# Kernel optimization log

Measured on AMD Instinct MI355X. Metric: run time of the kernel, lower is better.

## Reference

```python
import jax, jax.numpy as jnp
import numpy as np

B, T, D, KDIM = 256, 512, 256, 256

def setup_inputs() -> dict:
    key = jax.random.key(0)
    k1, k2, k3 = jax.random.split(key, 3)
    inputs = jax.random.normal(k1, (B, T, D), dtype=jnp.float32)
    # glorot-style scaling for stability of the recurrence
    U = jax.random.normal(k2, (D, KDIM), dtype=jnp.float32) * (1.0 / np.sqrt(D))
    W = jax.random.normal(k3, (KDIM, KDIM), dtype=jnp.float32) * (1.0 / np.sqrt(KDIM))
    b = jnp.zeros((KDIM,), dtype=jnp.float32)
    return {"inputs": inputs, "U": U, "W": W, "b": b}

def reference(inputs, U, W, b):
    # vanilla RNN: h_t = tanh(x_t U + h_{t-1} W + b); returns final hidden state
    xU = jnp.einsum('btd,dk->btk', inputs, U) + b  # precompute input projection [B,T,K]

    def step(h, xu_t):
        h = jnp.tanh(xu_t + h @ W)
        return h, None

    h0 = jnp.zeros((inputs.shape[0], W.shape[0]), dtype=inputs.dtype)
    h_final, _ = jax.lax.scan(step, h0, jnp.swapaxes(xU, 0, 1))  # scan over time
    # original keras code keeps a singleton time axis on the state: [B,1,K]
    return h_final[:, None, :]
```

## Files before the change

### kernel.cpp

```cpp
#include <hip/hip_runtime.h>
#include <hip/hip_bf16.h>


typedef _Float16 half8_t __attribute__((ext_vector_type(8)));
typedef _Float16 half2_t __attribute__((ext_vector_type(2)));
typedef float    float4_t __attribute__((ext_vector_type(4)));

#define MFMA16(a, b, c) __builtin_amdgcn_mfma_f32_16x16x32_f16((a), (b), (c), 0, 0, 0)

__device__ __forceinline__ half2_t pk_h2(float a, float b) {
    auto r = __builtin_amdgcn_cvt_pkrtz(a, b);
    return __builtin_bit_cast(half2_t, r);
}

__device__ __forceinline__ float fast_tanh(float x) {
    float e = __builtin_amdgcn_exp2f(2.8853900817779268f * x);
    return 1.0f - 2.0f * __builtin_amdgcn_rcpf(e + 1.0f);
}

__device__ __forceinline__ void lds_barrier() {
    __builtin_amdgcn_sched_barrier(0);
    asm volatile("s_waitcnt lgkmcnt(0)" ::: "memory");
    __builtin_amdgcn_s_barrier();
    __builtin_amdgcn_sched_barrier(0);
}

__global__ void transpose_u(const float* __restrict__ U, _Float16* __restrict__ Ut) {
    int id = blockIdx.x * 256 + threadIdx.x;
    int d = id >> 8, n = id & 255;
    Ut[n * 264 + d] = (_Float16)U[id];
}

__global__ __launch_bounds__(256, 3) void xu_gemm(
    const float* __restrict__ x,
    const _Float16* __restrict__ Ut,
    const float* __restrict__ bias,
    half2_t* __restrict__ xu)
{
    __shared__ char lds[40960];
    const int tid = threadIdx.x;
    const int lane = tid & 63, w = tid >> 6, l15 = lane & 15, q = lane >> 4;
    const int bx = blockIdx.x;
    const int m_tile = (bx & 7) | ((bx >> 4) << 3);
    const int n0 = ((bx >> 3) & 1) * 128;
    const size_t m0 = (size_t)m_tile * 128;

    float4 ar[4];
    uint4  br[2];

    auto loadA = [&](int it) {
#pragma unroll
        for (int i = 0; i < 4; ++i) {
            int u = tid + 256 * i, row = u >> 3, seg = u & 7;
            ar[i] = *(const float4*)(x + (m0 + row) * 256 + it * 32 + seg * 4);
        }
    };
    auto loadB = [&](int it) {
#pragma unroll
        for (int i = 0; i < 2; ++i) {
            int u = tid + 256 * i, p = u >> 2, seg = u & 3;
            int c = n0 + 32 * (p >> 5) + 2 * (p & 15) + ((p >> 4) & 1);
            br[i] = *(const uint4*)((const char*)Ut + c * 528 + it * 64 + seg * 16);
        }
    };
    auto writeAB = [&](int s) {
        char* As = lds + s * 10240;
        char* Bs = lds + 20480 + s * 10240;
#pragma unroll
        for (int i = 0; i < 4; ++i) {
            int u = tid + 256 * i, row = u >> 3, seg = u & 7;
            half2_t p0 = pk_h2(ar[i].x, ar[i].y);
            half2_t p1 = pk_h2(ar[i].z, ar[i].w);
            uint2 v;
            v.x = __builtin_bit_cast(unsigned, p0);
            v.y = __builtin_bit_cast(unsigned, p1);
            *(uint2*)(As + row * 80 + seg * 8) = v;
        }
#pragma unroll
        for (int i = 0; i < 2; ++i) {
            int u = tid + 256 * i, p = u >> 2, seg = u & 3;
            *(uint4*)(Bs + p * 80 + seg * 16) = br[i];
        }
    };

    float4_t acc[16];
#pragma unroll
    for (int i = 0; i < 16; ++i) { acc[i][0] = 0.f; acc[i][1] = 0.f; acc[i][2] = 0.f; acc[i][3] = 0.f; }

    loadA(0); loadB(0); writeAB(0);
    __syncthreads();

    for (int it = 0; it < 8; ++it) {
        if (it < 7) { loadA(it + 1); loadB(it + 1); }
        const char* As = lds + (it & 1) * 10240;
        const char* Bs = lds + 20480 + (it & 1) * 10240;
        half8_t af[2];
#pragma unroll
        for (int ms = 0; ms < 2; ++ms)
            af[ms] = *(const half8_t*)(As + (32 * w + 16 * ms + l15) * 80 + q * 16);
#pragma unroll
        for (int ns = 0; ns < 8; ++ns) {
            half8_t bf = *(const half8_t*)(Bs + (16 * ns + l15) * 80 + q * 16);
            acc[ns * 2 + 0] = MFMA16(af[0], bf, acc[ns * 2 + 0]);
            acc[ns * 2 + 1] = MFMA16(af[1], bf, acc[ns * 2 + 1]);
        }
        if (it < 7) writeAB((it + 1) & 1);
        __syncthreads();
    }

#pragma unroll
    for (int ms = 0; ms < 2; ++ms)
#pragma unroll
        for (int j = 0; j < 4; ++j) {
            const int c = n0 + 32 * j + 2 * l15;
            const float2 bb = *(const float2*)(bias + c);
#pragma unroll
            for (int i = 0; i < 4; ++i) {
                float v0 = acc[(2 * j) * 2 + ms][i] + bb.x;
                float v1 = acc[(2 * j + 1) * 2 + ms][i] + bb.y;
                half2_t p = pk_h2(v0, v1);
                int m_g = (int)m0 + 32 * w + 16 * ms + q * 4 + i;
                xu[(size_t)m_g * 128 + (c >> 1)] = p;
            }
        }
}

__global__ __launch_bounds__(512, 2) void rnn_scan(
    const half2_t* __restrict__ xu,
    const float* __restrict__ W,
    float* __restrict__ out)
{
    __shared__ char lds[16896];
    const int tid = threadIdx.x;
    const int lane = tid & 63, w = tid >> 6, l15 = lane & 15, q = lane >> 4;
    const int blk = blockIdx.x;
    const int c0 = 32 * w + 2 * l15;

    half8_t wf[2][8];
#pragma unroll
    for (int tt = 0; tt < 2; ++tt)
#pragma unroll
        for (int c = 0; c < 8; ++c) {
            half8_t f;
#pragma unroll
            for (int j = 0; j < 8; ++j) {
                int k = 32 * c + q * 8 + j;
                f[j] = (_Float16)W[k * 256 + c0 + tt];
            }
            wf[tt][c] = f;
        }

    for (int i = tid; i < 16896 / 4; i += 512) ((int*)lds)[i] = 0;

    const int rowg0 = 16 * blk + q * 4;
    const int colh = c0 >> 1;

    unsigned xoff[4];
#pragma unroll
    for (int i = 0; i < 4; ++i)
        xoff[i] = (unsigned)(rowg0 + i) * 512u * 128u + (unsigned)colh;

    half2_t xr[4][4];
#pragma unroll
    for (int p = 0; p < 4; ++p)
#pragma unroll
        for (int i = 0; i < 4; ++i)
            xr[p][i] = xu[xoff[i] + (unsigned)p * 128u];
#pragma unroll
    for (int i = 0; i < 4; ++i) xoff[i] += 512u;

    char* const L = (char*)lds;
    const int afb = l15 * 528 + q * 16;
    const int hwb = (q * 4) * 528 + c0 * 2;

    __syncthreads();

#define SCAN_STEP(P_, PAR, DOPF, LAST)                                          \
    {                                                                           \
        const char* hcur = L + ((PAR) ? 8448 : 0);                              \
        half8_t af[8];                                                          \
        _Pragma("unroll")                                                       \
        for (int c8 = 0; c8 < 8; ++c8)                                          \
            af[c8] = *(const half8_t*)(hcur + afb + c8 * 64);                   \
        float4_t a0a, a1a, a0b, a1b;                                            \
        _Pragma("unroll")                                                       \
        for (int i = 0; i < 4; ++i) {                                           \
            a0a[i] = (float)xr[P_][i][0];                                       \
            a1a[i] = (float)xr[P_][i][1];                                       \
            a0b[i] = 0.f; a1b[i] = 0.f;                                         \
        }                                                                       \
        if (DOPF) {                                                             \
            _Pragma("unroll")                                                   \
            for (int i = 0; i < 4; ++i) {                                       \
                xr[P_][i] = xu[xoff[i]];                                        \
                xoff[i] += 128u;                                                \
            }                                                                   \
        }                                                                       \
        _Pragma("unroll")                                                       \
        for (int c = 0; c < 4; ++c) {                                           \
            a0a = MFMA16(af[2 * c],     wf[0][2 * c],     a0a);                 \
            a1a = MFMA16(af[2 * c],     wf[1][2 * c],     a1a);                 \
            a0b = MFMA16(af[2 * c + 1], wf[0][2 * c + 1], a0b);                 \
            a1b = MFMA16(af[2 * c + 1], wf[1][2 * c + 1], a1b);                 \
        }                                                                       \
        if (LAST) {                                                             \
            _Pragma("unroll")                                                   \
            for (int i = 0; i < 4; ++i) {                                       \
                float2 st;                                                      \
                st.x = fast_tanh(a0a[i] + a0b[i]);                              \
                st.y = fast_tanh(a1a[i] + a1b[i]);                              \
                *(float2*)(&out[(rowg0 + i) * 256 + c0]) = st;                  \
            }                                                                   \
        } else {                                                                \
            char* hnext = L + ((PAR) ? 0 : 8448);                               \
            _Pragma("unroll")                                                   \
            for (int i = 0; i < 4; ++i) {                                       \
                float v0 = fast_tanh(a0a[i] + a0b[i]);                          \
                float v1 = fast_tanh(a1a[i] + a1b[i]);                          \
                *(half2_t*)(hnext + hwb + i * 528) = pk_h2(v0, v1);             \
            }                                                                   \
            lds_barrier();                                                      \
        }                                                                       \
    }

    for (int t4 = 0; t4 < 508; t4 += 4) {
        SCAN_STEP(0, 0, 1, 0)
        SCAN_STEP(1, 1, 1, 0)
        SCAN_STEP(2, 0, 1, 0)
        SCAN_STEP(3, 1, 1, 0)
    }
    SCAN_STEP(0, 0, 0, 0)
    SCAN_STEP(1, 1, 0, 0)
    SCAN_STEP(2, 0, 0, 0)
    SCAN_STEP(3, 1, 0, 1)
#undef SCAN_STEP
}

extern "C" void kernel_launch(void* const* d_in, const int* in_sizes, int n_in,
                              void* d_out, int out_size, void* d_ws, size_t ws_size,
                              hipStream_t stream) {
    const float* x = (const float*)d_in[0];
    const float* U = (const float*)d_in[1];
    const float* W = (const float*)d_in[2];
    const float* b = (const float*)d_in[3];
    float* out = (float*)d_out;

    char* ws = (char*)d_ws;
    _Float16* Ut = (_Float16*)ws;
    half2_t*  xu = (half2_t*)(ws + 262144);

    transpose_u<<<256, 256, 0, stream>>>(U, Ut);
    xu_gemm<<<2048, 256, 0, stream>>>(x, Ut, b, xu);
    rnn_scan<<<16, 512, 0, stream>>>(xu, W, out);
}
```

Measured before the change: 523.4 us.

## Fuse projection GEMM and RNN scan into one kernel with flag-based time-chunk overlap

Merges the U transpose, the xU projection GEMM and the recurrent scan into a single persistent launch. Blocks 0-15 run the scan while the remaining blocks compute xU in time-quarter chunks, publishing progress through global atomic flags so the scan can start once the first quarter is ready. The GEMM blocks now cover 128 rows x 256 columns each, sharing one A tile across two 256-thread halves. The aim is to hide the GEMM and launch gaps behind the serial scan, at the cost of spin-wait synchronisation and a reliance on all blocks being co-resident or scheduled in order to avoid deadlock.

```diff
diff --git a/kernel.cpp b/kernel.cpp
--- a/kernel.cpp
+++ b/kernel.cpp
@@ -25,155 +25,91 @@
     __builtin_amdgcn_sched_barrier(0);
 }
 
-__global__ void transpose_u(const float* __restrict__ U, _Float16* __restrict__ Ut) {
-    int id = blockIdx.x * 256 + threadIdx.x;
-    int d = id >> 8, n = id & 255;
-    Ut[n * 264 + d] = (_Float16)U[id];
-}
-
-__global__ __launch_bounds__(256, 3) void xu_gemm(
+__device__ __forceinline__ void wait_flag(unsigned* f, unsigned target) {
+    if (threadIdx.x == 0) {
+        while (__hip_atomic_load(f, __ATOMIC_ACQUIRE, __HIP_MEMORY_SCOPE_AGENT) < target)
+            __builtin_amdgcn_s_sleep(16);
+    }
+    __builtin_amdgcn_sched_barrier(0);
+    __builtin_amdgcn_s_barrier();
+    __builtin_amdgcn_sched_barrier(0);
+    asm volatile("" ::: "memory");
+}
+
+__global__ __launch_bounds__(512, 2) void fused(
     const float* __restrict__ x,
-    const _Float16* __restrict__ Ut,
+    const float* __restrict__ U,
+    const float* __restrict__ W,
     const float* __restrict__ bias,
-    half2_t* __restrict__ xu)
-{
-    __shared__ char lds[40960];
-    const int tid = threadIdx.x;
-    const int lane = tid & 63, w = tid >> 6, l15 = lane & 15, q = lane >> 4;
-    const int bx = blockIdx.x;
-    const int m_tile = (bx & 7) | ((bx >> 4) << 3);
-    const int n0 = ((bx >> 3) & 1) * 128;
-    const size_t m0 = (size_t)m_tile * 128;
-
-    float4 ar[4];
-    uint4  br[2];
-
-    auto loadA = [&](int it) {
-#pragma unroll
-        for (int i = 0; i < 4; ++i) {
-            int u = tid + 256 * i, row = u >> 3, seg = u & 7;
-            ar[i] = *(const float4*)(x + (m0 + row) * 256 + it * 32 + seg * 4);
-        }
-    };
-    auto loadB = [&](int it) {
-#pragma unroll
-        for (int i = 0; i < 2; ++i) {
-            int u = tid + 256 * i, p = u >> 2, seg = u & 3;
-            int c = n0 + 32 * (p >> 5) + 2 * (p & 15) + ((p >> 4) & 1);
-            br[i] = *(const uint4*)((const char*)Ut + c * 528 + it * 64 + seg * 16);
-        }
-    };
-    auto writeAB = [&](int s) {
-        char* As = lds + s * 10240;
-        char* Bs = lds + 20480 + s * 10240;
-#pragma unroll
-        for (int i = 0; i < 4; ++i) {
-            int u = tid + 256 * i, row = u >> 3, seg = u & 7;
-            half2_t p0 = pk_h2(ar[i].x, ar[i].y);
-            half2_t p1 = pk_h2(ar[i].z, ar[i].w);
-            uint2 v;
-            v.x = __builtin_bit_cast(unsigned, p0);
-            v.y = __builtin_bit_cast(unsigned, p1);
-            *(uint2*)(As + row * 80 + seg * 8) = v;
-        }
-#pragma unroll
-        for (int i = 0; i < 2; ++i) {
-            int u = tid + 256 * i, p = u >> 2, seg = u & 3;
-            *(uint4*)(Bs + p * 80 + seg * 16) = br[i];
-        }
-    };
-
-    float4_t acc[16];
-#pragma unroll
-    for (int i = 0; i < 16; ++i) { acc[i][0] = 0.f; acc[i][1] = 0.f; acc[i][2] = 0.f; acc[i][3] = 0.f; }
-
-    loadA(0); loadB(0); writeAB(0);
-    __syncthreads();
-
-    for (int it = 0; it < 8; ++it) {
-        if (it < 7) { loadA(it + 1); loadB(it + 1); }
-        const char* As = lds + (it & 1) * 10240;
-        const char* Bs = lds + 20480 + (it & 1) * 10240;
-        half8_t af[2];
-#pragma unroll
-        for (int ms = 0; ms < 2; ++ms)
-            af[ms] = *(const half8_t*)(As + (32 * w + 16 * ms + l15) * 80 + q * 16);
-#pragma unroll
-        for (int ns = 0; ns < 8; ++ns) {
-            half8_t bf = *(const half8_t*)(Bs + (16 * ns + l15) * 80 + q * 16);
-            acc[ns * 2 + 0] = MFMA16(af[0], bf, acc[ns * 2 + 0]);
-            acc[ns * 2 + 1] = MFMA16(af[1], bf, acc[ns * 2 + 1]);
-        }
-        if (it < 7) writeAB((it + 1) & 1);
-        __syncthreads();
-    }
-
-#pragma unroll
-    for (int ms = 0; ms < 2; ++ms)
-#pragma unroll
-        for (int j = 0; j < 4; ++j) {
-            const int c = n0 + 32 * j + 2 * l15;
-            const float2 bb = *(const float2*)(bias + c);
-#pragma unroll
-            for (int i = 0; i < 4; ++i) {
-                float v0 = acc[(2 * j) * 2 + ms][i] + bb.x;
-                float v1 = acc[(2 * j + 1) * 2 + ms][i] + bb.y;
-                half2_t p = pk_h2(v0, v1);
-                int m_g = (int)m0 + 32 * w + 16 * ms + q * 4 + i;
-                xu[(size_t)m_g * 128 + (c >> 1)] = p;
-            }
-        }
-}
-
-__global__ __launch_bounds__(512, 2) void rnn_scan(
-    const half2_t* __restrict__ xu,
-    const float* __restrict__ W,
+    _Float16* __restrict__ Ut,
+    half2_t* __restrict__ xu,
+    unsigned* __restrict__ flags,
     float* __restrict__ out)
 {
-    __shared__ char lds[16896];
+    __shared__ char lds[61440];
     const int tid = threadIdx.x;
-    const int lane = tid & 63, w = tid >> 6, l15 = lane & 15, q = lane >> 4;
-    const int blk = blockIdx.x;
-    const int c0 = 32 * w + 2 * l15;
-
-    half8_t wf[2][8];
-#pragma unroll
-    for (int tt = 0; tt < 2; ++tt)
-#pragma unroll
-        for (int c = 0; c < 8; ++c) {
-            half8_t f;
-#pragma unroll
-            for (int j = 0; j < 8; ++j) {
-                int k = 32 * c + q * 8 + j;
-                f[j] = (_Float16)W[k * 256 + c0 + tt];
-            }
-            wf[tt][c] = f;
-        }
-
-    for (int i = tid; i < 16896 / 4; i += 512) ((int*)lds)[i] = 0;
-
-    const int rowg0 = 16 * blk + q * 4;
-    const int colh = c0 >> 1;
-
-    unsigned xoff[4];
-#pragma unroll
-    for (int i = 0; i < 4; ++i)
-        xoff[i] = (unsigned)(rowg0 + i) * 512u * 128u + (unsigned)colh;
-
-    half2_t xr[4][4];
-#pragma unroll
-    for (int p = 0; p < 4; ++p)
+
+    if (blockIdx.x < 16) {
+        const int lane = tid & 63, w8 = tid >> 6, l15 = lane & 15, q4 = lane >> 4;
+        const int blk = blockIdx.x;
+        const int c0 = 32 * w8 + 2 * l15;
+
+        {
+            int idx = blk * 512 + tid;
+            const float4* up = (const float4*)U + (size_t)idx * 2;
+            float4 u0 = up[0], u1 = up[1];
+            int d = idx >> 5, n = (idx & 31) * 8;
+            _Float16* dst = Ut + (size_t)n * 264 + d;
+            dst[0 * 264] = (_Float16)u0.x;  dst[1 * 264] = (_Float16)u0.y;
+            dst[2 * 264] = (_Float16)u0.z;  dst[3 * 264] = (_Float16)u0.w;
+            dst[4 * 264] = (_Float16)u1.x;  dst[5 * 264] = (_Float16)u1.y;
+            dst[6 * 264] = (_Float16)u1.z;  dst[7 * 264] = (_Float16)u1.w;
+        }
+        __syncthreads();
+        if (tid == 0)
+            __hip_atomic_fetch_add(&flags[0], 1u, __ATOMIC_RELEASE,
+                                   __HIP_MEMORY_SCOPE_AGENT);
+
+        half8_t wf[2][8];
+#pragma unroll
+        for (int tt = 0; tt < 2; ++tt)
+#pragma unroll
+            for (int c = 0; c < 8; ++c) {
+                half8_t f;
+#pragma unroll
+                for (int j = 0; j < 8; ++j) {
+                    int k = 32 * c + q4 * 8 + j;
+                    f[j] = (_Float16)W[k * 256 + c0 + tt];
+                }
+                wf[tt][c] = f;
+            }
+
+        for (int i = tid; i < 16896 / 4; i += 512) ((int*)lds)[i] = 0;
+
+        const int rowg0 = 16 * blk + q4 * 4;
+        const int colh = c0 >> 1;
+
+        unsigned xoff[4];
 #pragma unroll
         for (int i = 0; i < 4; ++i)
-            xr[p][i] = xu[xoff[i] + (unsigned)p * 128u];
-#pragma unroll
-    for (int i = 0; i < 4; ++i) xoff[i] += 512u;
-
-    char* const L = (char*)lds;
-    const int afb = l15 * 528 + q * 16;
-    const int hwb = (q * 4) * 528 + c0 * 2;
-
-    __syncthreads();
+            xoff[i] = (unsigned)(rowg0 + i) * 512u * 128u + (unsigned)colh;
+
+        wait_flag(&flags[1], 256);
+
+        half2_t xr[4][4];
+#pragma unroll
+        for (int p = 0; p < 4; ++p)
+#pragma unroll
+            for (int i = 0; i < 4; ++i)
+                xr[p][i] = xu[xoff[i] + (unsigned)p * 128u];
+#pragma unroll
+        for (int i = 0; i < 4; ++i) xoff[i] += 512u;
+
+        char* const L = (char*)lds;
+        const int afb = l15 * 528 + q4 * 16;
+        const int hwb = (q4 * 4) * 528 + c0 * 2;
+
+        __syncthreads();
 
 #define SCAN_STEP(P_, PAR, DOPF, LAST)                                          \
     {                                                                           \
@@ -223,17 +159,121 @@
         }                                                                       \
     }
 
-    for (int t4 = 0; t4 < 508; t4 += 4) {
-        SCAN_STEP(0, 0, 1, 0)
-        SCAN_STEP(1, 1, 1, 0)
-        SCAN_STEP(2, 0, 1, 0)
-        SCAN_STEP(3, 1, 1, 0)
+        for (int t4 = 0; t4 < 508; t4 += 4) {
+            if ((t4 & 127) == 124) wait_flag(&flags[2 + (t4 >> 7)], 256);
+            SCAN_STEP(0, 0, 1, 0)
+            SCAN_STEP(1, 1, 1, 0)
+            SCAN_STEP(2, 0, 1, 0)
+            SCAN_STEP(3, 1, 1, 0)
+        }
+        SCAN_STEP(0, 0, 0, 0)
+        SCAN_STEP(1, 1, 0, 0)
+        SCAN_STEP(2, 0, 0, 0)
+        SCAN_STEP(3, 1, 0, 1)
+#undef SCAN_STEP
+
+    } else {
+        const int g  = blockIdx.x - 16;
+        const int qt = g >> 8;
+        const int bb = g & 255;
+        const size_t m0 = ((size_t)bb * 4 + qt) * 128;
+        const int h  = tid >> 8;
+        const int tl = tid & 255;
+        const int n0 = h * 128;
+        const int lane = tl & 63, w = tl >> 6, l15 = lane & 15, q4 = lane >> 4;
+
+        wait_flag(&flags[0], 16);
+
+        char* const As0 = lds;
+        char* const Bs0 = lds + 20480 + h * 20480;
+
+        float4 ar[4];
+        uint4  br[2];
+
+        auto loadA = [&](int it) {
+            if (h == 0) {
+#pragma unroll
+                for (int i = 0; i < 4; ++i) {
+                    int u = tl + 256 * i, row = u >> 3, sg = u & 7;
+                    ar[i] = *(const float4*)(x + (m0 + row) * 256 + it * 32 + sg * 4);
+                }
+            }
+        };
+        auto loadB = [&](int it) {
+#pragma unroll
+            for (int i = 0; i < 2; ++i) {
+                int u = tl + 256 * i, p = u >> 2, sg = u & 3;
+                int c = n0 + 32 * (p >> 5) + 2 * (p & 15) + ((p >> 4) & 1);
+                br[i] = *(const uint4*)((const char*)Ut + c * 528 + it * 64 + sg * 16);
+            }
+        };
+        auto writeAB = [&](int s) {
+            if (h == 0) {
+                char* As = As0 + s * 10240;
+#pragma unroll
+                for (int i = 0; i < 4; ++i) {
+                    int u = tl + 256 * i, row = u >> 3, sg = u & 7;
+                    uint2 v;
+                    v.x = __builtin_bit_cast(unsigned, pk_h2(ar[i].x, ar[i].y));
+                    v.y = __builtin_bit_cast(unsigned, pk_h2(ar[i].z, ar[i].w));
+                    *(uint2*)(As + row * 80 + sg * 8) = v;
+                }
+            }
+            char* Bs = Bs0 + s * 10240;
+#pragma unroll
+            for (int i = 0; i < 2; ++i) {
+                int u = tl + 256 * i, p = u >> 2, sg = u & 3;
+                *(uint4*)(Bs + p * 80 + sg * 16) = br[i];
+            }
+        };
+
+        float4_t acc[16];
+#pragma unroll
+        for (int i = 0; i < 16; ++i) {
+            acc[i][0] = 0.f; acc[i][1] = 0.f; acc[i][2] = 0.f; acc[i][3] = 0.f;
+        }
+
+        loadA(0); loadB(0); writeAB(0);
+        __syncthreads();
+
+        for (int it = 0; it < 8; ++it) {
+            if (it < 7) { loadA(it + 1); loadB(it + 1); }
+            const char* As = As0 + (it & 1) * 10240;
+            const char* Bs = Bs0 + (it & 1) * 10240;
+            half8_t af[2];
+#pragma unroll
+            for (int ms = 0; ms < 2; ++ms)
+                af[ms] = *(const half8_t*)(As + (32 * w + 16 * ms + l15) * 80 + q4 * 16);
+#pragma unroll
+            for (int ns = 0; ns < 8; ++ns) {
+                half8_t bf = *(const half8_t*)(Bs + (16 * ns + l15) * 80 + q4 * 16);
+                acc[ns * 2 + 0] = MFMA16(af[0], bf, acc[ns * 2 + 0]);
+                acc[ns * 2 + 1] = MFMA16(af[1], bf, acc[ns * 2 + 1]);
+            }
+            if (it < 7) writeAB((it + 1) & 1);
+            __syncthreads();
+        }
+
+#pragma unroll
+        for (int ms = 0; ms < 2; ++ms)
+#pragma unroll
+            for (int j = 0; j < 4; ++j) {
+                const int c = n0 + 32 * j + 2 * l15;
+                const float2 bv = *(const float2*)(bias + c);
+#pragma unroll
+                for (int i = 0; i < 4; ++i) {
+                    float v0 = acc[(2 * j) * 2 + ms][i] + bv.x;
+                    float v1 = acc[(2 * j + 1) * 2 + ms][i] + bv.y;
+                    int m_g = (int)m0 + 32 * w + 16 * ms + q4 * 4 + i;
+                    xu[(size_t)m_g * 128 + (c >> 1)] = pk_h2(v0, v1);
+                }
+            }
+
+        __syncthreads();
+        if (tid == 0)
+            __hip_atomic_fetch_add(&flags[1 + qt], 1u, __ATOMIC_RELEASE,
+                                   __HIP_MEMORY_SCOPE_AGENT);
     }
-    SCAN_STEP(0, 0, 0, 0)
-    SCAN_STEP(1, 1, 0, 0)
-    SCAN_STEP(2, 0, 0, 0)
-    SCAN_STEP(3, 1, 0, 1)
-#undef SCAN_STEP
 }
 
 extern "C" void kernel_launch(void* const* d_in, const int* in_sizes, int n_in,
@@ -246,10 +286,10 @@
     float* out = (float*)d_out;
 
     char* ws = (char*)d_ws;
-    _Float16* Ut = (_Float16*)ws;
-    half2_t*  xu = (half2_t*)(ws + 262144);
-
-    transpose_u<<<256, 256, 0, stream>>>(U, Ut);
-    xu_gemm<<<2048, 256, 0, stream>>>(x, Ut, b, xu);
-    rnn_scan<<<16, 512, 0, stream>>>(xu, W, out);
-}
+    _Float16* Ut   = (_Float16*)ws;
+    unsigned* flags = (unsigned*)(ws + 196608);
+    half2_t*  xu   = (half2_t*)(ws + 262144);
+
+    hipMemsetAsync(flags, 0, 64, stream);
+    fused<<<1040, 512, 0, stream>>>(x, U, W, b, Ut, xu, flags, out);
+}
```

Result: slower. 539.7 us (+3.1%).
